# Kernel tuning notes

Hardware: AMD Instinct MI355X
Metric: run time of the kernel (lower is better)

Reference implementation:

```python
import jax, jax.numpy as jnp
import numpy as np

NUM_NODES = 100000
NUM_EDGES = 3_200_000
WALKS_PER_NODE = 4
WALK_LENGTH = 8
SKIP_FIRST = True


def setup_inputs() -> dict:
    key = jax.random.key(0)
    k1, k2, k3 = jax.random.split(key, 3)
    edge_index = jax.random.randint(k1, (2, NUM_EDGES), 0, NUM_NODES, dtype=jnp.int32)
    edge_weight = jax.random.uniform(k2, (NUM_EDGES,), dtype=jnp.float32)
    # one uniform per walker per step; S = NUM_NODES * WALKS_PER_NODE
    rand_unif = jax.random.uniform(k3, (NUM_NODES * WALKS_PER_NODE, WALK_LENGTH), dtype=jnp.float32)
    return {"edge_index": edge_index, "edge_weight": edge_weight, "rand_unif": rand_unif}


def _random_walk_edges(edge_index, rand_unif):
    """Returns added [2, S*L] edges (root -> walked node), int dtype."""
    row, col = edge_index[0], edge_index[1]
    # is_sorted=False path: sort edges by source to build CSR
    order = jnp.argsort(row)
    row_s = row[order]
    col_s = col[order]
    deg = jax.ops.segment_sum(jnp.ones_like(row_s), row_s, num_segments=NUM_NODES)  # [N]
    rowptr = jnp.concatenate([jnp.zeros((1,), deg.dtype), jnp.cumsum(deg)])  # [N+1]
    # start = all nodes, repeated walks_per_node times
    start = jnp.tile(jnp.arange(NUM_NODES, dtype=row.dtype), WALKS_PER_NODE)  # [S]

    def step(cur, u):
        d = deg[cur]  # [S]
        off = jnp.minimum((u * d.astype(u.dtype)).astype(cur.dtype), jnp.maximum(d - 1, 0))
        nxt = jnp.where(d > 0, col_s[rowptr[cur] + off], cur)  # stay if isolated
        return nxt, nxt

    _, walks = jax.lax.scan(step, start, rand_unif.T)  # [L_total, S]
    walks = walks.T  # [S, WALK_LENGTH] == n_id[:, 1:]
    k = 1 if SKIP_FIRST else 0  # skip_first drops the first-hop node (n_id[:, 2:])
    targets = walks[:, k:]  # [S, L]
    L = targets.shape[1]
    roots = jnp.broadcast_to(start[:, None], (start.shape[0], L))
    return jnp.stack([roots.reshape(-1), targets.reshape(-1)])  # [2, S*L]


def reference(edge_index, edge_weight, rand_unif):
    added = _random_walk_edges(edge_index, rand_unif)
    out_edge_index = jnp.concatenate([edge_index, added], axis=1)
    added_w = jnp.ones((added.shape[1],), edge_weight.dtype)
    out_edge_weight = jnp.concatenate([edge_weight, added_w])
    return out_edge_index, out_edge_weight
```

## Files before the change

kernel.cpp:

```cpp
#include <hip/hip_runtime.h>

#define ARW_N_NODES   100000
#define ARW_N_EDGES   3200000
#define ARW_N_WALKERS 400000
#define ARW_WLEN      8
#define ARW_LOUT      7
#define ARW_ROW_LEN   6000000
#define ARW_OUT_ELEMS 18000000

#define ARW_NB    196
#define ARW_NT    3125
#define ARW_TP    3136
#define ARW_TILE  1024

#define ARW_HT    0
#define ARW_BT    700000
#define ARW_TOT   1350000
#define ARW_CB    1360000
#define ARW_PD    1400000
#define ARW_P     6000000
#define ARW_COLS  12000000

__global__ void AddRandomWalkEdge_16896401342869_kernel() {}

__global__ __launch_bounds__(1024) void arw16896_thist(const int* __restrict__ row,
                                                       int* __restrict__ s) {
    __shared__ int h[256];
    int tid = threadIdx.x;
    if (tid < 256) h[tid] = 0;
    __syncthreads();
    atomicAdd(&h[row[blockIdx.x * ARW_TILE + tid] >> 9], 1);
    __syncthreads();
    if (tid < ARW_NB) s[ARW_HT + tid * ARW_TP + blockIdx.x] = h[tid];
}

__global__ __launch_bounds__(1024) void arw16896_btot(int* __restrict__ s) {
    __shared__ int wsum[16];
    int b = blockIdx.x, tid = threadIdx.x, lane = tid & 63, wid = tid >> 6;
    int acc = 0;
    for (int t = tid; t < ARW_NT; t += 1024) acc += s[ARW_HT + b * ARW_TP + t];
    #pragma unroll
    for (int off = 32; off > 0; off >>= 1) acc += __shfl_down(acc, off, 64);
    if (lane == 0) wsum[wid] = acc;
    __syncthreads();
    if (tid == 0) {
        int a = 0;
        #pragma unroll
        for (int w = 0; w < 16; w++) a += wsum[w];
        s[ARW_TOT + b] = a;
    }
}

__global__ __launch_bounds__(256) void arw16896_bbase(int* __restrict__ s) {
    __shared__ int sm[256];
    int tid = threadIdx.x;
    int v = (tid < ARW_NB) ? s[ARW_TOT + tid] : 0;
    sm[tid] = v;
    __syncthreads();
    for (int off = 1; off < 256; off <<= 1) {
        int x = 0;
        if (tid >= off) x = sm[tid - off];
        __syncthreads();
        sm[tid] += x;
        __syncthreads();
    }
    if (tid < ARW_NB) s[ARW_CB + tid] = sm[tid] - v;
}

__global__ __launch_bounds__(1024) void arw16896_bscan2(int* __restrict__ s) {
    __shared__ int wsum[16];
    int b = blockIdx.x, tid = threadIdx.x, lane = tid & 63, wid = tid >> 6;
    int carry = s[ARW_CB + b];
    for (int c0 = 0; c0 < ARW_NT; c0 += 1024) {
        int t = c0 + tid;
        int v = (t < ARW_NT) ? s[ARW_HT + b * ARW_TP + t] : 0;
        int sv = v;
        #pragma unroll
        for (int off = 1; off < 64; off <<= 1) {
            int x = __shfl_up(sv, off, 64);
            if (lane >= off) sv += x;
        }
        if (lane == 63) wsum[wid] = sv;
        __syncthreads();
        int pre = 0, tot = 0;
        #pragma unroll
        for (int w = 0; w < 16; w++) {
            int x = wsum[w];
            if (w < wid) pre += x;
            tot += x;
        }
        if (t < ARW_NT) s[ARW_BT + b * ARW_TP + t] = carry + pre + sv - v;
        carry += tot;
        __syncthreads();
    }
}

__global__ __launch_bounds__(1024) void arw16896_part(const int* __restrict__ row,
                                                      const int* __restrict__ col,
                                                      int* __restrict__ s) {
    __shared__ unsigned W[16 * 256];
    int tid  = threadIdx.x;
    int wave = tid >> 6, lane = tid & 63;
    int e = blockIdx.x * ARW_TILE + tid;
    int r = row[e], cv = col[e];
    int b = r >> 9;
    W[tid] = 0; W[tid + 1024] = 0; W[tid + 2048] = 0; W[tid + 3072] = 0;
    __syncthreads();
    unsigned long long mask = ~0ULL;
    #pragma unroll
    for (int bit = 0; bit < 8; bit++) {
        unsigned long long bal = __ballot((b >> bit) & 1);
        mask &= ((b >> bit) & 1) ? bal : ~bal;
    }
    int rankw = __popcll(mask & ((1ULL << lane) - 1ULL));
    W[wave * 256 + b] = (unsigned)__popcll(mask);
    __syncthreads();
    int cross = 0;
    for (int w2 = 0; w2 < 16; w2++) {
        if (w2 >= wave) break;
        cross += (int)W[w2 * 256 + b];
    }
    int base = s[ARW_BT + b * ARW_TP + blockIdx.x];
    s[ARW_P + base + cross + rankw] = ((r & 511) << 17) | cv;
}

__global__ __launch_bounds__(1024) void arw16896_pass2(int* __restrict__ s) {
    __shared__ unsigned W[16 * 512];
    __shared__ int hist[512], pref[512], runc[512];
    int tid = threadIdx.x, lane = tid & 63, wave = tid >> 6;
    int b = blockIdx.x;
    int start = s[ARW_BT + b * ARW_TP];
    int end   = (b == ARW_NB - 1) ? ARW_N_EDGES : s[ARW_BT + (b + 1) * ARW_TP];
    int cnt = end - start;
    int rows0 = b << 9;
    int nrows = ARW_N_NODES - rows0; if (nrows > 512) nrows = 512;

    if (tid < 512) hist[tid] = 0;
    __syncthreads();
    for (int k = tid; k < cnt; k += 1024)
        atomicAdd(&hist[(unsigned)s[ARW_P + start + k] >> 17], 1);
    __syncthreads();
    if (tid < 512) pref[tid] = hist[tid];
    __syncthreads();
    for (int off = 1; off < 512; off <<= 1) {
        int x = 0;
        if (tid < 512 && tid >= off) x = pref[tid - off];
        __syncthreads();
        if (tid < 512) pref[tid] += x;
        __syncthreads();
    }
    if (tid < 512) runc[tid] = 0;
    if (tid < nrows) {
        unsigned deg = (unsigned)hist[tid];
        unsigned rp  = (unsigned)(start + pref[tid] - hist[tid]);
        s[ARW_PD + rows0 + tid] = (int)((rp << 10) | deg);
    }
    __syncthreads();

    for (int c0 = 0; c0 < cnt; c0 += 1024) {
        int k = c0 + tid;
        int valid = (k < cnt) ? 1 : 0;
        unsigned p = valid ? (unsigned)s[ARW_P + start + k] : 0u;
        unsigned lr = p >> 17;
        #pragma unroll
        for (int j = 0; j < 8; j++) W[tid + j * 1024] = 0;
        __syncthreads();
        unsigned long long mask = ~0ULL;
        #pragma unroll
        for (int bit = 0; bit < 9; bit++) {
            unsigned long long bal = __ballot((lr >> bit) & 1u);
            mask &= ((lr >> bit) & 1u) ? bal : ~bal;
        }
        mask &= __ballot(valid);
        int rankw = __popcll(mask & ((1ULL << lane) - 1ULL));
        if (valid) W[wave * 512 + lr] = (unsigned)__popcll(mask);
        __syncthreads();
        if (valid) {
            int cross = 0;
            for (int w2 = 0; w2 < 16; w2++) {
                if (w2 >= wave) break;
                cross += (int)W[w2 * 512 + lr];
            }
            int pos = start + (pref[lr] - hist[lr]) + runc[lr] + cross + rankw;
            s[ARW_COLS + pos] = (int)(p & 0x1FFFFu);
        }
        __syncthreads();
        if (tid < 512) {
            int a = 0;
            #pragma unroll
            for (int w = 0; w < 16; w++) a += (int)W[w * 512 + tid];
            runc[tid] += a;
        }
        __syncthreads();
    }
}

__global__ __launch_bounds__(256) void arw16896_walk(const float* __restrict__ ru,
                                                     const int* __restrict__ s,
                                                     float* __restrict__ o) {
    __shared__ float tg[4 * 256 * ARW_LOUT];
    int tid = threadIdx.x;
    int v = blockIdx.x * 256 + tid;
    if (v < ARW_N_NODES) {
        float uu[4][8];
        int cur[4];
        #pragma unroll
        for (int k = 0; k < 4; k++) {
            const float4* rp4 = (const float4*)(ru + (size_t)(v + k * ARW_N_NODES) * 8);
            float4 ra = rp4[0], rb = rp4[1];
            uu[k][0] = ra.x; uu[k][1] = ra.y; uu[k][2] = ra.z; uu[k][3] = ra.w;
            uu[k][4] = rb.x; uu[k][5] = rb.y; uu[k][6] = rb.z; uu[k][7] = rb.w;
        }
        unsigned pd0 = (unsigned)s[ARW_PD + v];
        int d0  = (int)(pd0 & 1023u);
        int rp0 = (int)(pd0 >> 10);
        #pragma unroll
        for (int k = 0; k < 4; k++) {
            int off = (int)(uu[k][0] * (float)d0);
            if (off > d0 - 1) off = d0 - 1;
            int nxt = s[ARW_COLS + rp0 + off];
            cur[k] = (d0 > 0) ? nxt : v;
        }
        #pragma unroll
        for (int t = 1; t < ARW_WLEN; t++) {
            unsigned pdk[4];
            #pragma unroll
            for (int k = 0; k < 4; k++) pdk[k] = (unsigned)s[ARW_PD + cur[k]];
            #pragma unroll
            for (int k = 0; k < 4; k++) {
                int d = (int)(pdk[k] & 1023u);
                int off = (int)(uu[k][t] * (float)d);
                if (off > d - 1) off = d - 1;
                int nxt = s[ARW_COLS + (int)(pdk[k] >> 10) + off];
                cur[k] = (d > 0) ? nxt : cur[k];
                tg[k * (256 * ARW_LOUT) + tid * ARW_LOUT + (t - 1)] = (float)cur[k];
            }
        }
    }
    __syncthreads();
    int blkN = ARW_N_NODES - blockIdx.x * 256;
    if (blkN > 256) blkN = 256;
    int valid = blkN * ARW_LOUT;
    #pragma unroll
    for (int k = 0; k < 4; k++) {
        int base = ARW_ROW_LEN + ARW_N_EDGES +
                   (k * ARW_N_NODES + blockIdx.x * 256) * ARW_LOUT;
        for (int j = tid; j < valid; j += 256)
            o[base + j] = tg[k * (256 * ARW_LOUT) + j];
    }
}

__global__ __launch_bounds__(256) void arw16896_asm(const int* __restrict__ ei,
                                                    const float* __restrict__ wgt,
                                                    float* __restrict__ o) {
    int i4 = blockIdx.x * blockDim.x + threadIdx.x;
    if (i4 < ARW_N_EDGES / 4) {
        int4 r0 = ((const int4*)ei)[i4];
        int4 r1 = ((const int4*)(ei + ARW_N_EDGES))[i4];
        float4 wv = ((const float4*)wgt)[i4];
        ((float4*)o)[i4] = make_float4((float)r0.x, (float)r0.y, (float)r0.z, (float)r0.w);
        ((float4*)(o + ARW_ROW_LEN))[i4] =
            make_float4((float)r1.x, (float)r1.y, (float)r1.z, (float)r1.w);
        ((float4*)(o + 2 * ARW_ROW_LEN))[i4] = wv;
    }
    if (i4 < (ARW_N_WALKERS * ARW_LOUT) / 4) {
        int i = i4 * 4;
        float4 r;
        r.x = (float)(((i    ) / ARW_LOUT) % ARW_N_NODES);
        r.y = (float)(((i + 1) / ARW_LOUT) % ARW_N_NODES);
        r.z = (float)(((i + 2) / ARW_LOUT) % ARW_N_NODES);
        r.w = (float)(((i + 3) / ARW_LOUT) % ARW_N_NODES);
        ((float4*)(o + ARW_N_EDGES))[i4] = r;
        ((float4*)(o + 2 * ARW_ROW_LEN + ARW_N_EDGES))[i4] = make_float4(1.f, 1.f, 1.f, 1.f);
    }
}

extern "C" void kernel_launch(void* const* d_in, const int* in_sizes, int n_in,
                              void* d_out, int out_size, void* d_ws, size_t ws_size,
                              hipStream_t stream) {
    const int*   ei  = (const int*)d_in[0];
    const float* wgt = (const float*)d_in[1];
    const float* ru  = (const float*)d_in[2];
    int*   s = (int*)d_out;
    float* o = (float*)d_out;
    const int* row = ei;
    const int* col = ei + ARW_N_EDGES;

    arw16896_thist <<<ARW_NT, 1024, 0, stream>>>(row, s);
    arw16896_btot  <<<ARW_NB, 1024, 0, stream>>>(s);
    arw16896_bbase <<<1, 256, 0, stream>>>(s);
    arw16896_bscan2<<<ARW_NB, 1024, 0, stream>>>(s);
    arw16896_part  <<<ARW_NT, 1024, 0, stream>>>(row, col, s);
    arw16896_pass2 <<<ARW_NB, 1024, 0, stream>>>(s);
    arw16896_walk  <<<(ARW_N_NODES + 255) / 256, 256, 0, stream>>>(ru, s, o);
    arw16896_asm   <<<(ARW_N_EDGES / 4 + 255) / 256, 256, 0, stream>>>(ei, wgt, o);
}
```

Before: 247.2 us.

## Build CSR via global atomic degree count, scatter, and per-row stable rank sort

Replaces the two-level stable radix partition (tile histograms, block scans, bucket partition, in-bucket ballot ranking) with a counting-sort CSR build. It takes per-node degrees with global atomics, scans them to get row pointers, and scatters (edge id, col) pairs with atomic slot claims. Each row is then stably ordered by edge id with a per-wave rank sort. This cuts the multi-pass ballot and shared-memory work, but adds heavy global atomic contention, an 8-byte scatter buffer, and a quadratic fallback for rows with more than 64 edges.

```diff
diff --git a/kernel.cpp b/kernel.cpp
--- a/kernel.cpp
+++ b/kernel.cpp
@@ -8,190 +8,119 @@
 #define ARW_ROW_LEN   6000000
 #define ARW_OUT_ELEMS 18000000
 
-#define ARW_NB    196
-#define ARW_NT    3125
-#define ARW_TP    3136
-#define ARW_TILE  1024
-
-#define ARW_HT    0
-#define ARW_BT    700000
-#define ARW_TOT   1350000
-#define ARW_CB    1360000
+#define ARW_DEG   0
+#define ARW_CNT   150000
+#define ARW_TOT   300000
+#define ARW_CB2   300200
 #define ARW_PD    1400000
-#define ARW_P     6000000
+#define ARW_EC    2600000
 #define ARW_COLS  12000000
 
+#define ARW_NC2   98
+
 __global__ void AddRandomWalkEdge_16896401342869_kernel() {}
 
-__global__ __launch_bounds__(1024) void arw16896_thist(const int* __restrict__ row,
-                                                       int* __restrict__ s) {
-    __shared__ int h[256];
+__global__ __launch_bounds__(1024) void arw16896_zero(int* __restrict__ s) {
+    int i = blockIdx.x * 1024 + threadIdx.x;
+    if (i < ARW_N_NODES) s[ARW_DEG + i] = 0;
+}
+
+__global__ __launch_bounds__(256) void arw16896_deg(const int* __restrict__ row,
+                                                    int* __restrict__ s) {
+    int e = blockIdx.x * 256 + threadIdx.x;
+    atomicAdd(&s[ARW_DEG + row[e]], 1);
+}
+
+__global__ __launch_bounds__(1024) void arw16896_tot(int* __restrict__ s) {
+    __shared__ int wsum[16];
+    int j = blockIdx.x, tid = threadIdx.x, lane = tid & 63, wid = tid >> 6;
+    int idx = j * 1024 + tid;
+    int a = (idx < ARW_N_NODES) ? s[ARW_DEG + idx] : 0;
+    #pragma unroll
+    for (int off = 32; off > 0; off >>= 1) a += __shfl_down(a, off, 64);
+    if (lane == 0) wsum[wid] = a;
+    __syncthreads();
+    if (tid == 0) {
+        int t = 0;
+        #pragma unroll
+        for (int w = 0; w < 16; w++) t += wsum[w];
+        s[ARW_TOT + j] = t;
+    }
+}
+
+__global__ __launch_bounds__(128) void arw16896_base(int* __restrict__ s) {
+    __shared__ int sm[128];
     int tid = threadIdx.x;
-    if (tid < 256) h[tid] = 0;
-    __syncthreads();
-    atomicAdd(&h[row[blockIdx.x * ARW_TILE + tid] >> 9], 1);
-    __syncthreads();
-    if (tid < ARW_NB) s[ARW_HT + tid * ARW_TP + blockIdx.x] = h[tid];
-}
-
-__global__ __launch_bounds__(1024) void arw16896_btot(int* __restrict__ s) {
-    __shared__ int wsum[16];
-    int b = blockIdx.x, tid = threadIdx.x, lane = tid & 63, wid = tid >> 6;
-    int acc = 0;
-    for (int t = tid; t < ARW_NT; t += 1024) acc += s[ARW_HT + b * ARW_TP + t];
-    #pragma unroll
-    for (int off = 32; off > 0; off >>= 1) acc += __shfl_down(acc, off, 64);
-    if (lane == 0) wsum[wid] = acc;
-    __syncthreads();
-    if (tid == 0) {
-        int a = 0;
-        #pragma unroll
-        for (int w = 0; w < 16; w++) a += wsum[w];
-        s[ARW_TOT + b] = a;
-    }
-}
-
-__global__ __launch_bounds__(256) void arw16896_bbase(int* __restrict__ s) {
-    __shared__ int sm[256];
-    int tid = threadIdx.x;
-    int v = (tid < ARW_NB) ? s[ARW_TOT + tid] : 0;
+    int v = (tid < ARW_NC2) ? s[ARW_TOT + tid] : 0;
     sm[tid] = v;
     __syncthreads();
-    for (int off = 1; off < 256; off <<= 1) {
+    for (int off = 1; off < 128; off <<= 1) {
         int x = 0;
         if (tid >= off) x = sm[tid - off];
         __syncthreads();
         sm[tid] += x;
         __syncthreads();
     }
-    if (tid < ARW_NB) s[ARW_CB + tid] = sm[tid] - v;
-}
-
-__global__ __launch_bounds__(1024) void arw16896_bscan2(int* __restrict__ s) {
+    if (tid < ARW_NC2) s[ARW_CB2 + tid] = sm[tid] - v;
+}
+
+__global__ __launch_bounds__(1024) void arw16896_ptr(int* __restrict__ s) {
     __shared__ int wsum[16];
-    int b = blockIdx.x, tid = threadIdx.x, lane = tid & 63, wid = tid >> 6;
-    int carry = s[ARW_CB + b];
-    for (int c0 = 0; c0 < ARW_NT; c0 += 1024) {
-        int t = c0 + tid;
-        int v = (t < ARW_NT) ? s[ARW_HT + b * ARW_TP + t] : 0;
-        int sv = v;
-        #pragma unroll
-        for (int off = 1; off < 64; off <<= 1) {
-            int x = __shfl_up(sv, off, 64);
-            if (lane >= off) sv += x;
-        }
-        if (lane == 63) wsum[wid] = sv;
-        __syncthreads();
-        int pre = 0, tot = 0;
-        #pragma unroll
-        for (int w = 0; w < 16; w++) {
-            int x = wsum[w];
-            if (w < wid) pre += x;
-            tot += x;
-        }
-        if (t < ARW_NT) s[ARW_BT + b * ARW_TP + t] = carry + pre + sv - v;
-        carry += tot;
-        __syncthreads();
-    }
-}
-
-__global__ __launch_bounds__(1024) void arw16896_part(const int* __restrict__ row,
-                                                      const int* __restrict__ col,
-                                                      int* __restrict__ s) {
-    __shared__ unsigned W[16 * 256];
-    int tid  = threadIdx.x;
-    int wave = tid >> 6, lane = tid & 63;
-    int e = blockIdx.x * ARW_TILE + tid;
-    int r = row[e], cv = col[e];
-    int b = r >> 9;
-    W[tid] = 0; W[tid + 1024] = 0; W[tid + 2048] = 0; W[tid + 3072] = 0;
-    __syncthreads();
-    unsigned long long mask = ~0ULL;
+    int j = blockIdx.x, tid = threadIdx.x, lane = tid & 63, wid = tid >> 6;
+    int idx = j * 1024 + tid;
+    int v = (idx < ARW_N_NODES) ? s[ARW_DEG + idx] : 0;
+    int sv = v;
     #pragma unroll
-    for (int bit = 0; bit < 8; bit++) {
-        unsigned long long bal = __ballot((b >> bit) & 1);
-        mask &= ((b >> bit) & 1) ? bal : ~bal;
-    }
-    int rankw = __popcll(mask & ((1ULL << lane) - 1ULL));
-    W[wave * 256 + b] = (unsigned)__popcll(mask);
-    __syncthreads();
-    int cross = 0;
-    for (int w2 = 0; w2 < 16; w2++) {
-        if (w2 >= wave) break;
-        cross += (int)W[w2 * 256 + b];
-    }
-    int base = s[ARW_BT + b * ARW_TP + blockIdx.x];
-    s[ARW_P + base + cross + rankw] = ((r & 511) << 17) | cv;
-}
-
-__global__ __launch_bounds__(1024) void arw16896_pass2(int* __restrict__ s) {
-    __shared__ unsigned W[16 * 512];
-    __shared__ int hist[512], pref[512], runc[512];
-    int tid = threadIdx.x, lane = tid & 63, wave = tid >> 6;
-    int b = blockIdx.x;
-    int start = s[ARW_BT + b * ARW_TP];
-    int end   = (b == ARW_NB - 1) ? ARW_N_EDGES : s[ARW_BT + (b + 1) * ARW_TP];
-    int cnt = end - start;
-    int rows0 = b << 9;
-    int nrows = ARW_N_NODES - rows0; if (nrows > 512) nrows = 512;
-
-    if (tid < 512) hist[tid] = 0;
-    __syncthreads();
-    for (int k = tid; k < cnt; k += 1024)
-        atomicAdd(&hist[(unsigned)s[ARW_P + start + k] >> 17], 1);
-    __syncthreads();
-    if (tid < 512) pref[tid] = hist[tid];
-    __syncthreads();
-    for (int off = 1; off < 512; off <<= 1) {
-        int x = 0;
-        if (tid < 512 && tid >= off) x = pref[tid - off];
-        __syncthreads();
-        if (tid < 512) pref[tid] += x;
-        __syncthreads();
-    }
-    if (tid < 512) runc[tid] = 0;
-    if (tid < nrows) {
-        unsigned deg = (unsigned)hist[tid];
-        unsigned rp  = (unsigned)(start + pref[tid] - hist[tid]);
-        s[ARW_PD + rows0 + tid] = (int)((rp << 10) | deg);
-    }
-    __syncthreads();
-
-    for (int c0 = 0; c0 < cnt; c0 += 1024) {
-        int k = c0 + tid;
-        int valid = (k < cnt) ? 1 : 0;
-        unsigned p = valid ? (unsigned)s[ARW_P + start + k] : 0u;
-        unsigned lr = p >> 17;
-        #pragma unroll
-        for (int j = 0; j < 8; j++) W[tid + j * 1024] = 0;
-        __syncthreads();
-        unsigned long long mask = ~0ULL;
-        #pragma unroll
-        for (int bit = 0; bit < 9; bit++) {
-            unsigned long long bal = __ballot((lr >> bit) & 1u);
-            mask &= ((lr >> bit) & 1u) ? bal : ~bal;
-        }
-        mask &= __ballot(valid);
-        int rankw = __popcll(mask & ((1ULL << lane) - 1ULL));
-        if (valid) W[wave * 512 + lr] = (unsigned)__popcll(mask);
-        __syncthreads();
-        if (valid) {
-            int cross = 0;
-            for (int w2 = 0; w2 < 16; w2++) {
-                if (w2 >= wave) break;
-                cross += (int)W[w2 * 512 + lr];
-            }
-            int pos = start + (pref[lr] - hist[lr]) + runc[lr] + cross + rankw;
-            s[ARW_COLS + pos] = (int)(p & 0x1FFFFu);
-        }
-        __syncthreads();
-        if (tid < 512) {
-            int a = 0;
-            #pragma unroll
-            for (int w = 0; w < 16; w++) a += (int)W[w * 512 + tid];
-            runc[tid] += a;
-        }
-        __syncthreads();
+    for (int off = 1; off < 64; off <<= 1) {
+        int x = __shfl_up(sv, off, 64);
+        if (lane >= off) sv += x;
+    }
+    if (lane == 63) wsum[wid] = sv;
+    __syncthreads();
+    int pre = 0;
+    for (int w = 0; w < wid; w++) pre += wsum[w];
+    if (idx < ARW_N_NODES) {
+        unsigned rb = (unsigned)(s[ARW_CB2 + j] + pre + sv - v);
+        s[ARW_PD + idx]  = (int)((rb << 10) | (unsigned)v);
+        s[ARW_CNT + idx] = (int)rb;
+    }
+}
+
+__global__ __launch_bounds__(256) void arw16896_scat(const int* __restrict__ row,
+                                                     const int* __restrict__ col,
+                                                     int* __restrict__ s) {
+    int e = blockIdx.x * 256 + threadIdx.x;
+    int r = row[e], c = col[e];
+    int pos = atomicAdd(&s[ARW_CNT + r], 1);
+    ((int2*)(s + ARW_EC))[pos] = make_int2(e, c);
+}
+
+__global__ __launch_bounds__(256) void arw16896_rsort(int* __restrict__ s) {
+    int tid = threadIdx.x, lane = tid & 63;
+    int r = blockIdx.x * 4 + (tid >> 6);
+    if (r >= ARW_N_NODES) return;
+    unsigned pdv = (unsigned)s[ARW_PD + r];
+    int d    = (int)(pdv & 1023u);
+    int base = (int)(pdv >> 10);
+    if (d == 0) return;
+    const int2* ec = (const int2*)(s + ARW_EC);
+    if (d <= 64) {
+        int2 me = ec[base + lane];
+        int ex = me.x;
+        int rk = 0;
+        #pragma unroll
+        for (int j = 0; j < 64; j++) {
+            int ej = __shfl(ex, j, 64);
+            rk += (j < d && j != lane && ej < ex) ? 1 : 0;
+        }
+        if (lane < d) s[ARW_COLS + base + rk] = me.y;
+    } else {
+        for (int ii = lane; ii < d; ii += 64) {
+            int2 me = ec[base + ii];
+            int rk = 0;
+            for (int j = 0; j < d; j++) rk += (ec[base + j].x < me.x) ? 1 : 0;
+            s[ARW_COLS + base + rk] = me.y;
+        }
     }
 }
 
@@ -286,12 +215,13 @@
     const int* row = ei;
     const int* col = ei + ARW_N_EDGES;
 
-    arw16896_thist <<<ARW_NT, 1024, 0, stream>>>(row, s);
-    arw16896_btot  <<<ARW_NB, 1024, 0, stream>>>(s);
-    arw16896_bbase <<<1, 256, 0, stream>>>(s);
-    arw16896_bscan2<<<ARW_NB, 1024, 0, stream>>>(s);
-    arw16896_part  <<<ARW_NT, 1024, 0, stream>>>(row, col, s);
-    arw16896_pass2 <<<ARW_NB, 1024, 0, stream>>>(s);
-    arw16896_walk  <<<(ARW_N_NODES + 255) / 256, 256, 0, stream>>>(ru, s, o);
-    arw16896_asm   <<<(ARW_N_EDGES / 4 + 255) / 256, 256, 0, stream>>>(ei, wgt, o);
-}
+    arw16896_zero <<<ARW_NC2, 1024, 0, stream>>>(s);
+    arw16896_deg  <<<ARW_N_EDGES / 256, 256, 0, stream>>>(row, s);
+    arw16896_tot  <<<ARW_NC2, 1024, 0, stream>>>(s);
+    arw16896_base <<<1, 128, 0, stream>>>(s);
+    arw16896_ptr  <<<ARW_NC2, 1024, 0, stream>>>(s);
+    arw16896_scat <<<ARW_N_EDGES / 256, 256, 0, stream>>>(row, col, s);
+    arw16896_rsort<<<(ARW_N_NODES + 3) / 4, 256, 0, stream>>>(s);
+    arw16896_walk <<<(ARW_N_NODES + 255) / 256, 256, 0, stream>>>(ru, s, o);
+    arw16896_asm  <<<(ARW_N_EDGES / 4 + 255) / 256, 256, 0, stream>>>(ei, wgt, o);
+}
```

Result: slower. 631.1 us (+155.3%).

## Replace ballot-based stable local sort with atomic scatter plus per-row rank sort

Applied to the files above, without the earlier changes.

The second pass of the CSR build no longer does a wave-ballot stable partition with four block barriers per 1024-element chunk. Instead it scatters each edge to its row bucket using shared-memory atomics, tagging it with its original index, and then restores the stable order inside each row with a per-wave rank sort. That sort uses shuffles for rows of at most 64 entries and a quadratic global-memory scan for larger rows. This removes most of the synchronisation, but adds a scratch buffer round trip and extra rank-computation work per row.

```diff
diff --git a/kernel.cpp b/kernel.cpp
--- a/kernel.cpp
+++ b/kernel.cpp
@@ -18,6 +18,7 @@
 #define ARW_TOT   1350000
 #define ARW_CB    1360000
 #define ARW_PD    1400000
+#define ARW_S2    2600000
 #define ARW_P     6000000
 #define ARW_COLS  12000000
 
@@ -125,19 +126,18 @@
 }
 
 __global__ __launch_bounds__(1024) void arw16896_pass2(int* __restrict__ s) {
-    __shared__ unsigned W[16 * 512];
-    __shared__ int hist[512], pref[512], runc[512];
-    int tid = threadIdx.x, lane = tid & 63, wave = tid >> 6;
+    __shared__ int hist[512], pref[512], cnt[512];
+    int tid = threadIdx.x;
     int b = blockIdx.x;
     int start = s[ARW_BT + b * ARW_TP];
     int end   = (b == ARW_NB - 1) ? ARW_N_EDGES : s[ARW_BT + (b + 1) * ARW_TP];
-    int cnt = end - start;
+    int ce = end - start;
     int rows0 = b << 9;
     int nrows = ARW_N_NODES - rows0; if (nrows > 512) nrows = 512;
 
-    if (tid < 512) hist[tid] = 0;
-    __syncthreads();
-    for (int k = tid; k < cnt; k += 1024)
+    if (tid < 512) { hist[tid] = 0; cnt[tid] = 0; }
+    __syncthreads();
+    for (int k = tid; k < ce; k += 1024)
         atomicAdd(&hist[(unsigned)s[ARW_P + start + k] >> 17], 1);
     __syncthreads();
     if (tid < 512) pref[tid] = hist[tid];
@@ -149,7 +149,6 @@
         if (tid < 512) pref[tid] += x;
         __syncthreads();
     }
-    if (tid < 512) runc[tid] = 0;
     if (tid < nrows) {
         unsigned deg = (unsigned)hist[tid];
         unsigned rp  = (unsigned)(start + pref[tid] - hist[tid]);
@@ -157,41 +156,41 @@
     }
     __syncthreads();
 
-    for (int c0 = 0; c0 < cnt; c0 += 1024) {
-        int k = c0 + tid;
-        int valid = (k < cnt) ? 1 : 0;
-        unsigned p = valid ? (unsigned)s[ARW_P + start + k] : 0u;
+    for (int k = tid; k < ce; k += 1024) {
+        unsigned p = (unsigned)s[ARW_P + start + k];
         unsigned lr = p >> 17;
-        #pragma unroll
-        for (int j = 0; j < 8; j++) W[tid + j * 1024] = 0;
-        __syncthreads();
-        unsigned long long mask = ~0ULL;
-        #pragma unroll
-        for (int bit = 0; bit < 9; bit++) {
-            unsigned long long bal = __ballot((lr >> bit) & 1u);
-            mask &= ((lr >> bit) & 1u) ? bal : ~bal;
-        }
-        mask &= __ballot(valid);
-        int rankw = __popcll(mask & ((1ULL << lane) - 1ULL));
-        if (valid) W[wave * 512 + lr] = (unsigned)__popcll(mask);
-        __syncthreads();
-        if (valid) {
-            int cross = 0;
-            for (int w2 = 0; w2 < 16; w2++) {
-                if (w2 >= wave) break;
-                cross += (int)W[w2 * 512 + lr];
+        int pos = atomicAdd(&cnt[lr], 1);
+        s[ARW_S2 + start + (pref[lr] - hist[lr]) + pos] =
+            (int)(((unsigned)k << 17) | (p & 0x1FFFFu));
+    }
+    __syncthreads();
+
+    int wave = tid >> 6, lane = tid & 63;
+    for (int rr = wave; rr < nrows; rr += 16) {
+        int d = hist[rr];
+        if (d == 0) continue;
+        int gbase = start + pref[rr] - hist[rr];
+        if (d <= 64) {
+            unsigned val = (unsigned)s[ARW_S2 + gbase + (lane < d ? lane : 0)];
+            int q = (int)(val >> 17);
+            int rk = 0;
+            #pragma unroll
+            for (int j = 0; j < 64; j++) {
+                int qj = __shfl(q, j, 64);
+                rk += (j < d && qj < q) ? 1 : 0;
             }
-            int pos = start + (pref[lr] - hist[lr]) + runc[lr] + cross + rankw;
-            s[ARW_COLS + pos] = (int)(p & 0x1FFFFu);
-        }
-        __syncthreads();
-        if (tid < 512) {
-            int a = 0;
-            #pragma unroll
-            for (int w = 0; w < 16; w++) a += (int)W[w * 512 + tid];
-            runc[tid] += a;
-        }
-        __syncthreads();
+            if (lane < d) s[ARW_COLS + gbase + rk] = (int)(val & 0x1FFFFu);
+        } else {
+            for (int ii = lane; ii < d; ii += 64) {
+                unsigned vi = (unsigned)s[ARW_S2 + gbase + ii];
+                int qi = (int)(vi >> 17), rk = 0;
+                for (int j = 0; j < d; j++) {
+                    unsigned vj = (unsigned)s[ARW_S2 + gbase + j];
+                    rk += ((int)(vj >> 17) < qi) ? 1 : 0;
+                }
+                s[ARW_COLS + gbase + rk] = (int)(vi & 0x1FFFFu);
+            }
+        }
     }
 }
 
```

Measured after the change: 335.2 us. +35.6%, slower.

## Compress CSR columns to 16-bit plus bitplane and batch histogram tiles per block

Applied to the files above, without the earlier changes.

Adds a conversion kernel that packs the sorted column array into 16-bit values plus a ballot-built bitmask for bit 16. The walk kernel then reconstructs node ids from the two, so its random gathers touch a smaller, more cache-friendly footprint. Separately, the tile histogram kernel now processes 25 tiles per block with per-tile shared histograms, cutting block count and launch overhead. The trade-off is an extra pass over 3.2M edges and two loads per gather instead of one.

```diff
diff --git a/kernel.cpp b/kernel.cpp
--- a/kernel.cpp
+++ b/kernel.cpp
@@ -12,12 +12,15 @@
 #define ARW_NT    3125
 #define ARW_TP    3136
 #define ARW_TILE  1024
+#define ARW_TPB   25
 
 #define ARW_HT    0
 #define ARW_BT    700000
 #define ARW_TOT   1350000
 #define ARW_CB    1360000
 #define ARW_PD    1400000
+#define ARW_C16   2600000
+#define ARW_BITS  4300000
 #define ARW_P     6000000
 #define ARW_COLS  12000000
 
@@ -25,13 +28,19 @@
 
 __global__ __launch_bounds__(1024) void arw16896_thist(const int* __restrict__ row,
                                                        int* __restrict__ s) {
-    __shared__ int h[256];
+    __shared__ int h[ARW_TPB * 256];
     int tid = threadIdx.x;
-    if (tid < 256) h[tid] = 0;
-    __syncthreads();
-    atomicAdd(&h[row[blockIdx.x * ARW_TILE + tid] >> 9], 1);
-    __syncthreads();
-    if (tid < ARW_NB) s[ARW_HT + tid * ARW_TP + blockIdx.x] = h[tid];
+    for (int x = tid; x < ARW_TPB * 256; x += 1024) h[x] = 0;
+    __syncthreads();
+    int base_e = blockIdx.x * (ARW_TPB * ARW_TILE) + tid;
+    #pragma unroll
+    for (int j = 0; j < ARW_TPB; j++)
+        atomicAdd(&h[j * 256 + (row[base_e + j * 1024] >> 9)], 1);
+    __syncthreads();
+    for (int x = tid; x < ARW_TPB * ARW_NB; x += 1024) {
+        int b = x / ARW_TPB, j = x % ARW_TPB;
+        s[ARW_HT + b * ARW_TP + blockIdx.x * ARW_TPB + j] = h[j * 256 + b];
+    }
 }
 
 __global__ __launch_bounds__(1024) void arw16896_btot(int* __restrict__ s) {
@@ -195,6 +204,15 @@
     }
 }
 
+__global__ __launch_bounds__(1024) void arw16896_cvt(int* __restrict__ s) {
+    int i = blockIdx.x * 1024 + threadIdx.x;
+    int lane = threadIdx.x & 63;
+    int c = s[ARW_COLS + i];
+    ((unsigned short*)(s + ARW_C16))[i] = (unsigned short)c;
+    unsigned long long hb = __ballot((c >> 16) & 1);
+    if (lane == 0) ((unsigned long long*)(s + ARW_BITS))[i >> 6] = hb;
+}
+
 __global__ __launch_bounds__(256) void arw16896_walk(const float* __restrict__ ru,
                                                      const int* __restrict__ s,
                                                      float* __restrict__ o) {
@@ -202,6 +220,8 @@
     int tid = threadIdx.x;
     int v = blockIdx.x * 256 + tid;
     if (v < ARW_N_NODES) {
+        const unsigned short* c16 = (const unsigned short*)(s + ARW_C16);
+        const unsigned long long* bp = (const unsigned long long*)(s + ARW_BITS);
         float uu[4][8];
         int cur[4];
         #pragma unroll
@@ -218,7 +238,8 @@
         for (int k = 0; k < 4; k++) {
             int off = (int)(uu[k][0] * (float)d0);
             if (off > d0 - 1) off = d0 - 1;
-            int nxt = s[ARW_COLS + rp0 + off];
+            int pos = rp0 + off;
+            int nxt = (int)c16[pos] | ((int)((bp[pos >> 6] >> (pos & 63)) & 1ULL) << 16);
             cur[k] = (d0 > 0) ? nxt : v;
         }
         #pragma unroll
@@ -231,7 +252,8 @@
                 int d = (int)(pdk[k] & 1023u);
                 int off = (int)(uu[k][t] * (float)d);
                 if (off > d - 1) off = d - 1;
-                int nxt = s[ARW_COLS + (int)(pdk[k] >> 10) + off];
+                int pos = (int)(pdk[k] >> 10) + off;
+                int nxt = (int)c16[pos] | ((int)((bp[pos >> 6] >> (pos & 63)) & 1ULL) << 16);
                 cur[k] = (d > 0) ? nxt : cur[k];
                 tg[k * (256 * ARW_LOUT) + tid * ARW_LOUT + (t - 1)] = (float)cur[k];
             }
@@ -286,12 +308,13 @@
     const int* row = ei;
     const int* col = ei + ARW_N_EDGES;
 
-    arw16896_thist <<<ARW_NT, 1024, 0, stream>>>(row, s);
+    arw16896_thist <<<ARW_NT / ARW_TPB, 1024, 0, stream>>>(row, s);
     arw16896_btot  <<<ARW_NB, 1024, 0, stream>>>(s);
     arw16896_bbase <<<1, 256, 0, stream>>>(s);
     arw16896_bscan2<<<ARW_NB, 1024, 0, stream>>>(s);
     arw16896_part  <<<ARW_NT, 1024, 0, stream>>>(row, col, s);
     arw16896_pass2 <<<ARW_NB, 1024, 0, stream>>>(s);
+    arw16896_cvt   <<<ARW_N_EDGES / 1024, 1024, 0, stream>>>(s);
     arw16896_walk  <<<(ARW_N_NODES + 255) / 256, 256, 0, stream>>>(ru, s, o);
     arw16896_asm   <<<(ARW_N_EDGES / 4 + 255) / 256, 256, 0, stream>>>(ei, wgt, o);
 }
```

Measured after the change: 263.4 us. +6.6%, slower.
